# Optimization experiments

Hardware: AMD Instinct MI355X
Metric: run time of the kernel (lower is better)

Reference implementation:

```python
import jax, jax.numpy as jnp
import numpy as np

EPS_NORM = 1e-12  # torch F.normalize default eps
EPS_OUT = 1e-06   # module eps
CLAMP = 100.0


def setup_inputs() -> dict:
    key = jax.random.key(0)
    kq, kk = jax.random.split(key)
    B, H, S, D = 2, 16, 2048, 128
    q = jax.random.normal(kq, (B, H, S, D), dtype=jnp.float32)
    k = jax.random.normal(kk, (B, H, S, D), dtype=jnp.float32)
    log_temperature = jnp.zeros((), dtype=jnp.float32)  # log(1.0)
    return {"q": q, "k": k, "log_temperature": log_temperature}


def _l2norm(x):
    # matches torch F.normalize: x / max(||x||_2, eps)
    n = jnp.sqrt(jnp.sum(x * x, axis=-1, keepdims=True))
    return x / jnp.maximum(n, EPS_NORM)


def reference(q, k, log_temperature):
    temp = jnp.clip(jnp.exp(log_temperature), 0.05, 100.0)
    qn = _l2norm(q)
    kn = _l2norm(k)
    # (B,H,S,D) x (B,H,S,D) -> (B,H,S,S)
    scores = jnp.einsum("bhsd,bhtd->bhst", qn, kn)
    scores = jnp.clip(scores / temp, -CLAMP, CLAMP)
    kernel = jnp.exp(scores)
    return kernel + EPS_OUT
```

## Files before the change

kernel.cpp:

```cpp
#include <hip/hip_runtime.h>

#define S 2048
#define D 128
#define BH 32
#define ROWS (BH * S)

typedef __bf16 bf16x8 __attribute__((ext_vector_type(8)));
typedef float f32x4 __attribute__((ext_vector_type(4)));
typedef __attribute__((address_space(1))) unsigned int GU;
typedef __attribute__((address_space(3))) unsigned int LU;

__device__ __forceinline__ unsigned short f2bf(float f) {
  unsigned u = __float_as_uint(f);
  u += 0x7fffu + ((u >> 16) & 1u);
  return (unsigned short)(u >> 16);
}

__device__ __forceinline__ void ld_g2l16(const unsigned short* g, unsigned short* l) {
  __builtin_amdgcn_global_load_lds((const GU*)g, (LU*)l, 16, 0, 0);
}

__global__ __launch_bounds__(256) void normalize_rows(
    const float* __restrict__ x, unsigned short* __restrict__ y) {
  const int wave = threadIdx.x >> 6;
  const int lane = threadIdx.x & 63;
  const int row = (blockIdx.x << 2) + wave;
  const float2 v = ((const float2*)(x + (size_t)row * D))[lane];
  float ss = v.x * v.x + v.y * v.y;
#pragma unroll
  for (int m = 32; m; m >>= 1) ss += __shfl_xor(ss, m, 64);
  const float scale = 1.0f / fmaxf(sqrtf(ss), 1e-12f);
  const unsigned lo = f2bf(v.x * scale);
  const unsigned hi = f2bf(v.y * scale);
  ((unsigned int*)(y + (size_t)row * D))[lane] = lo | (hi << 16);
}

__global__ __launch_bounds__(256, 2) void qk_exp_kernel(
    const unsigned short* __restrict__ Qn, const unsigned short* __restrict__ Kn,
    const float* __restrict__ logt, float* __restrict__ out) {
  __shared__ __align__(16) unsigned short lQ[128 * 128];
  __shared__ __align__(16) unsigned short lK[128 * 128];
  const int tid = threadIdx.x;
  const int nt_ = blockIdx.x, mt_ = blockIdx.y, bh = blockIdx.z;
  const unsigned short* Qb = Qn + ((size_t)bh * S + (size_t)mt_ * 128) * D;
  const unsigned short* Kb = Kn + ((size_t)bh * S + (size_t)nt_ * 128) * D;

#pragma unroll
  for (int it = 0; it < 8; ++it) {
    const int L = (it << 8) + tid;
    const int r = L >> 4, c = L & 15;
    const int g = (r << 4) + (c ^ (r & 15));
    ld_g2l16(Qb + (g << 3), lQ + (L << 3));
    ld_g2l16(Kb + (g << 3), lK + (L << 3));
  }
  __syncthreads();

  const int lane = tid & 63, wave = tid >> 6;
  const int wr = (wave >> 1) << 6;
  const int wc = (wave & 1) << 6;
  const int lm = lane & 15, kq = lane >> 4;

  f32x4 acc[4][4] = {};
#pragma unroll
  for (int ks = 0; ks < 4; ++ks) {
    const int kc = (ks << 2) + kq;
    const int sw = (kc ^ lm) << 3;
    bf16x8 a[4], b[4];
#pragma unroll
    for (int mt = 0; mt < 4; ++mt)
      a[mt] = *(const bf16x8*)(lQ + (wr + (mt << 4) + lm) * D + sw);
#pragma unroll
    for (int nt = 0; nt < 4; ++nt)
      b[nt] = *(const bf16x8*)(lK + (wc + (nt << 4) + lm) * D + sw);
#pragma unroll
    for (int mt = 0; mt < 4; ++mt)
#pragma unroll
      for (int nt = 0; nt < 4; ++nt)
        acc[mt][nt] =
            __builtin_amdgcn_mfma_f32_16x16x32_bf16(a[mt], b[nt], acc[mt][nt], 0, 0, 0);
  }

  float temp = __expf(logt[0]);
  temp = fminf(fmaxf(temp, 0.05f), 100.0f);
  const float invt = 1.0f / temp;

  float* Cb = out + ((size_t)bh << 22);
  const int rb = (mt_ << 7) + wr + (kq << 2);
  const int cb = (nt_ << 7) + wc + lm;
#pragma unroll
  for (int mt = 0; mt < 4; ++mt) {
#pragma unroll
    for (int reg = 0; reg < 4; ++reg) {
      const int row = rb + (mt << 4) + reg;
      float* rp = Cb + (size_t)row * S + cb;
#pragma unroll
      for (int nt = 0; nt < 4; ++nt) {
        float s = acc[mt][nt][reg] * invt;
        s = fminf(fmaxf(s, -100.0f), 100.0f);
        rp[nt << 4] = __expf(s) + 1e-6f;
      }
    }
  }
}

extern "C" void kernel_launch(void* const* d_in, const int* in_sizes, int n_in,
                              void* d_out, int out_size, void* d_ws, size_t ws_size,
                              hipStream_t stream) {
  const float* q = (const float*)d_in[0];
  const float* k = (const float*)d_in[1];
  const float* lt = (const float*)d_in[2];
  float* out = (float*)d_out;
  unsigned short* qn = (unsigned short*)d_ws;
  unsigned short* kn = qn + (size_t)ROWS * D;
  normalize_rows<<<ROWS / 4, 256, 0, stream>>>(q, qn);
  normalize_rows<<<ROWS / 4, 256, 0, stream>>>(k, kn);
  dim3 grid(S / 128, S / 128, BH);
  qk_exp_kernel<<<grid, 256, 0, stream>>>(qn, kn, lt, out);
}
```

Baseline: 629.1 us.

## Load Q fragments directly from global and drop Q LDS tile to raise occupancy

The Q tile no longer goes through LDS. Each wave owns 32 rows and reads its A fragments straight from global memory, prefetching one k-step ahead, while only the K tile is staged in LDS. Halving LDS use and raising launch bounds to 4 blocks per CU are meant to raise occupancy and hide the latency of the output-bound store phase. The cost is uncoalesced 16-byte global reads for Q, and a wave layout of 2x8 tiles per wave that needs more B fragment reads from LDS.

```diff
diff --git a/kernel.cpp b/kernel.cpp
--- a/kernel.cpp
+++ b/kernel.cpp
@@ -35,10 +35,9 @@
   ((unsigned int*)(y + (size_t)row * D))[lane] = lo | (hi << 16);
 }
 
-__global__ __launch_bounds__(256, 2) void qk_exp_kernel(
+__global__ __launch_bounds__(256, 4) void qk_exp_kernel(
     const unsigned short* __restrict__ Qn, const unsigned short* __restrict__ Kn,
     const float* __restrict__ logt, float* __restrict__ out) {
-  __shared__ __align__(16) unsigned short lQ[128 * 128];
   __shared__ __align__(16) unsigned short lK[128 * 128];
   const int tid = threadIdx.x;
   const int nt_ = blockIdx.x, mt_ = blockIdx.y, bh = blockIdx.z;
@@ -50,34 +49,39 @@
     const int L = (it << 8) + tid;
     const int r = L >> 4, c = L & 15;
     const int g = (r << 4) + (c ^ (r & 15));
-    ld_g2l16(Qb + (g << 3), lQ + (L << 3));
     ld_g2l16(Kb + (g << 3), lK + (L << 3));
   }
+
+  const int lane = tid & 63, wave = tid >> 6;
+  const int wr = wave << 5;
+  const int lm = lane & 15, kq = lane >> 4;
+
+  const unsigned short* qrow0 = Qb + (size_t)(wr + lm) * D + (kq << 3);
+
+  bf16x8 a0 = *(const bf16x8*)(qrow0);
+  bf16x8 a1 = *(const bf16x8*)(qrow0 + (D << 4));
   __syncthreads();
 
-  const int lane = tid & 63, wave = tid >> 6;
-  const int wr = (wave >> 1) << 6;
-  const int wc = (wave & 1) << 6;
-  const int lm = lane & 15, kq = lane >> 4;
-
-  f32x4 acc[4][4] = {};
+  f32x4 acc[2][8] = {};
 #pragma unroll
   for (int ks = 0; ks < 4; ++ks) {
+    const int ksn = (ks + 1) & 3;
+    bf16x8 a0n = *(const bf16x8*)(qrow0 + (ksn << 5));
+    bf16x8 a1n = *(const bf16x8*)(qrow0 + (D << 4) + (ksn << 5));
+
     const int kc = (ks << 2) + kq;
     const int sw = (kc ^ lm) << 3;
-    bf16x8 a[4], b[4];
+    bf16x8 b[8];
 #pragma unroll
-    for (int mt = 0; mt < 4; ++mt)
-      a[mt] = *(const bf16x8*)(lQ + (wr + (mt << 4) + lm) * D + sw);
+    for (int nt = 0; nt < 8; ++nt)
+      b[nt] = *(const bf16x8*)(lK + ((nt << 4) + lm) * D + sw);
 #pragma unroll
-    for (int nt = 0; nt < 4; ++nt)
-      b[nt] = *(const bf16x8*)(lK + (wc + (nt << 4) + lm) * D + sw);
-#pragma unroll
-    for (int mt = 0; mt < 4; ++mt)
-#pragma unroll
-      for (int nt = 0; nt < 4; ++nt)
-        acc[mt][nt] =
-            __builtin_amdgcn_mfma_f32_16x16x32_bf16(a[mt], b[nt], acc[mt][nt], 0, 0, 0);
+    for (int nt = 0; nt < 8; ++nt) {
+      acc[0][nt] = __builtin_amdgcn_mfma_f32_16x16x32_bf16(a0, b[nt], acc[0][nt], 0, 0, 0);
+      acc[1][nt] = __builtin_amdgcn_mfma_f32_16x16x32_bf16(a1, b[nt], acc[1][nt], 0, 0, 0);
+    }
+    a0 = a0n;
+    a1 = a1n;
   }
 
   float temp = __expf(logt[0]);
@@ -86,15 +90,15 @@
 
   float* Cb = out + ((size_t)bh << 22);
   const int rb = (mt_ << 7) + wr + (kq << 2);
-  const int cb = (nt_ << 7) + wc + lm;
+  const int cb = (nt_ << 7) + lm;
 #pragma unroll
-  for (int mt = 0; mt < 4; ++mt) {
+  for (int mt = 0; mt < 2; ++mt) {
 #pragma unroll
     for (int reg = 0; reg < 4; ++reg) {
       const int row = rb + (mt << 4) + reg;
       float* rp = Cb + (size_t)row * S + cb;
 #pragma unroll
-      for (int nt = 0; nt < 4; ++nt) {
+      for (int nt = 0; nt < 8; ++nt) {
         float s = acc[mt][nt][reg] * invt;
         s = fminf(fmaxf(s, -100.0f), 100.0f);
         rp[nt << 4] = __expf(s) + 1e-6f;
```

Result: no change. 630.7 us (+0.3%).
